# Performance work log

Measured on AMD Instinct MI355X. Metric: run time of the kernel, lower is better.

The kernel has to match this reference:

```python
import jax, jax.numpy as jnp
import numpy as np

HIDDEN = 1024
NUM_HEADS = 16
HEAD = HIDDEN // NUM_HEADS  # 64
LEFT = 64
RIGHT = 8
NUM_POS = LEFT + RIGHT + 1  # 73


def setup_inputs() -> dict:
    key = jax.random.key(0)
    ks = jax.random.split(key, 10)
    s = 1.0 / np.sqrt(HIDDEN)
    return {
        "hidden_states": jax.random.normal(ks[0], (4, 2048, HIDDEN), jnp.float32),
        "Wq": jax.random.normal(ks[1], (HIDDEN, HIDDEN), jnp.float32) * s,
        "bq": jax.random.normal(ks[2], (HIDDEN,), jnp.float32) * 0.01,
        "Wk": jax.random.normal(ks[3], (HIDDEN, HIDDEN), jnp.float32) * s,
        "bk": jax.random.normal(ks[4], (HIDDEN,), jnp.float32) * 0.01,
        "Wv": jax.random.normal(ks[5], (HIDDEN, HIDDEN), jnp.float32) * s,
        "bv": jax.random.normal(ks[6], (HIDDEN,), jnp.float32) * 0.01,
        "Wo": jax.random.normal(ks[7], (HIDDEN, HIDDEN), jnp.float32) * s,
        "bo": jax.random.normal(ks[8], (HIDDEN,), jnp.float32) * 0.01,
        "dist_emb": jax.random.normal(ks[9], (NUM_POS, HEAD), jnp.float32),
    }


def reference(hidden_states, Wq, bq, Wk, bk, Wv, bv, Wo, bo, dist_emb):
    B, L, H = hidden_states.shape
    scale = 1.0 / np.sqrt(HEAD)
    # projections (torch Linear: x @ W.T + b), reshape to [B, nH, L, d]
    def proj(W, b):
        return (hidden_states @ W.T + b).reshape(B, L, NUM_HEADS, HEAD).transpose(0, 2, 1, 3)
    q = proj(Wq, bq)
    k = proj(Wk, bk)
    v = proj(Wv, bv)
    attn = jnp.einsum('bhld,bhrd->bhlr', q, k) * scale  # [B,H,L,L]
    # relative-key positional bias
    dist = jnp.arange(L)[None, :] - jnp.arange(L)[:, None]  # r - l
    dist = jnp.clip(dist, -LEFT, RIGHT) + LEFT  # indices in [0, NUM_POS)
    pos_emb = dist_emb[dist]  # [L, L, d]
    rel = jnp.einsum('bhld,lrd->bhlr', q, pos_emb) * scale
    attn = jax.nn.softmax(attn + rel, axis=-1)
    out = jnp.einsum('bhlr,bhrd->bhld', attn, v)
    out = out.transpose(0, 2, 1, 3).reshape(B, L, H)
    return out @ Wo.T + bo
```

## Files before the change

kernel.cpp:

```cpp
#include <hip/hip_runtime.h>
#include <stdint.h>

#define SEQ   2048
#define BATCH 4
#define NH    16
#define HD    64
#define HID   1024
#define NPOS  73

typedef __attribute__((ext_vector_type(8))) short short8;
typedef __attribute__((ext_vector_type(4))) short short4v;
typedef __attribute__((ext_vector_type(4))) float f32x4;

static __device__ __forceinline__ float bf2f(short s) {
  return __uint_as_float(((unsigned)(unsigned short)s) << 16);
}
static __device__ __forceinline__ short f2bf(float f) {
  unsigned u = __float_as_uint(f);
  u += 0x7fffu + ((u >> 16) & 1u);
  return (short)(u >> 16);
}
static __device__ __forceinline__ unsigned pkbf(float a, float b) {
  unsigned d;
  asm("v_cvt_pk_bf16_f32 %0, %1, %2" : "=v"(d) : "v"(a), "v"(b));
  return d;
}

static __device__ __forceinline__ void gload_lds16(const void* g, void* lds) {
  __builtin_amdgcn_global_load_lds(
      (const __attribute__((address_space(1))) unsigned int*)g,
      (__attribute__((address_space(3))) unsigned int*)lds, 16, 0, 0);
}

__global__ __launch_bounds__(256) void cvt_kernel(const float* __restrict__ in,
                                                  short* __restrict__ out, int n4) {
  int i = blockIdx.x * 256 + threadIdx.x;
  if (i >= n4) return;
  f32x4 f = *(const f32x4*)(in + (long)i * 4);
  short4v o;
  o[0] = f2bf(f[0]); o[1] = f2bf(f[1]); o[2] = f2bf(f[2]); o[3] = f2bf(f[3]);
  *(short4v*)(out + (long)i * 4) = o;
}

__global__ __launch_bounds__(256) void cvt4_kernel(const float* __restrict__ a,
                                                   const float* __restrict__ b,
                                                   const float* __restrict__ c,
                                                   const float* __restrict__ d,
                                                   short* __restrict__ oa,
                                                   short* __restrict__ ob,
                                                   short* __restrict__ oc,
                                                   short* __restrict__ od, int n4) {
  int i = blockIdx.x * 256 + threadIdx.x;
  if (i >= n4) return;
  int m = blockIdx.y;
  const float* in = m == 0 ? a : m == 1 ? b : m == 2 ? c : d;
  short* out = m == 0 ? oa : m == 1 ? ob : m == 2 ? oc : od;
  f32x4 f = *(const f32x4*)(in + (long)i * 4);
  short4v o;
  o[0] = f2bf(f[0]); o[1] = f2bf(f[1]); o[2] = f2bf(f[2]); o[3] = f2bf(f[3]);
  *(short4v*)(out + (long)i * 4) = o;
}

template <int MODE>
__global__ __launch_bounds__(256) void gemm_nt(const short* __restrict__ A,
                                               const short* __restrict__ B,
                                               const float* __restrict__ bias,
                                               void* __restrict__ Cout, float scale) {
  __shared__ __align__(16) short As[128 * 32];
  __shared__ __align__(16) short Bs[128 * 32];
  const int K = HID;
  const f32x4 fzero = {0.f, 0.f, 0.f, 0.f};
  int t = threadIdx.x;
  int w = t >> 6, lane = t & 63;
  int wr = w >> 1, wc = w & 1;
  int g = lane >> 4, r = lane & 15;
  long tile_m = (long)blockIdx.x * 128;
  long tile_n = (long)blockIdx.y * 128;

  f32x4 acc[4][4];
#pragma unroll
  for (int m = 0; m < 4; ++m)
#pragma unroll
    for (int n = 0; n < 4; ++n) acc[m][n] = fzero;

  int e0 = w * 1024 + lane * 8;
  int e1 = e0 + 512;
  const short* A0 = A + (tile_m + (e0 >> 5)) * K + (e0 & 31);
  const short* A1 = A + (tile_m + (e1 >> 5)) * K + (e1 & 31);
  const short* B0 = B + (tile_n + (e0 >> 5)) * K + (e0 & 31);
  const short* B1 = B + (tile_n + (e1 >> 5)) * K + (e1 & 31);

  for (int k0 = 0; k0 < K; k0 += 32) {
    __syncthreads();
    gload_lds16(A0 + k0, &As[e0]);
    gload_lds16(A1 + k0, &As[e1]);
    gload_lds16(B0 + k0, &Bs[e0]);
    gload_lds16(B1 + k0, &Bs[e1]);
    __syncthreads();
    short8 af[4], bfr[4];
#pragma unroll
    for (int m = 0; m < 4; ++m)
      af[m] = *(const short8*)&As[(wr * 64 + m * 16 + r) * 32 + g * 8];
#pragma unroll
    for (int n = 0; n < 4; ++n)
      bfr[n] = *(const short8*)&Bs[(wc * 64 + n * 16 + r) * 32 + g * 8];
#pragma unroll
    for (int m = 0; m < 4; ++m)
#pragma unroll
      for (int n = 0; n < 4; ++n)
        acc[m][n] = __builtin_amdgcn_mfma_f32_16x16x32_bf16(af[m], bfr[n], acc[m][n], 0, 0, 0);
  }

#pragma unroll
  for (int m = 0; m < 4; ++m) {
    int row0 = (int)tile_m + wr * 64 + m * 16 + g * 4;
#pragma unroll
    for (int n = 0; n < 4; ++n) {
      int col = (int)tile_n + wc * 64 + n * 16 + r;
      float bs = bias[col];
#pragma unroll
      for (int j = 0; j < 4; ++j) {
        int row = row0 + j;
        float val = (acc[m][n][j] + bs) * scale;
        if (MODE == 0) {
          int b = row >> 11, l = row & (SEQ - 1);
          int hh = col >> 6, d = col & 63;
          ((short*)Cout)[(((long)(b * NH + hh) * SEQ + l) << 6) + d] = f2bf(val);
        } else if (MODE == 2) {
          int b = row >> 11, l = row & (SEQ - 1);
          int hh = col >> 6, d = col & 63;
          ((short*)Cout)[(((long)(b * NH + hh) * HD + d) << 11) + l] = f2bf(val);
        } else {
          ((float*)Cout)[(long)row * HID + col] = val;
        }
      }
    }
  }
}

__global__ __launch_bounds__(256, 3) void attn_kernel(const short* __restrict__ Qg,
                                                      const short* __restrict__ Kg,
                                                      const short* __restrict__ Vg,
                                                      const short* __restrict__ DE,
                                                      short* __restrict__ ctx) {
  __shared__ __align__(16) char arena[32768];
  __shared__ __align__(16) short qd2[128 * NPOS];

  short* Qs = (short*)arena;
  short* Ds = (short*)(arena + 16384);

  const f32x4 fzero = {0.f, 0.f, 0.f, 0.f};
  int t = threadIdx.x;
  int w = t >> 6, lane = t & 63;
  int g = lane >> 4, r = lane & 15;
  int h = blockIdx.x & (NH - 1), b = blockIdx.x >> 4, qt = blockIdx.y;
  int q0 = qt * 128;
  const short* Qp = Qg + ((long)(b * NH + h) * SEQ + q0) * HD;
  const short* Kp = Kg + (long)(b * NH + h) * SEQ * HD;
  const short* VTp = Vg + (long)(b * NH + h) * HD * SEQ;

#pragma unroll
  for (int c = 0; c < 4; ++c)
    gload_lds16(Qp + c * 2048 + t * 8, &Qs[c * 2048 + t * 8]);
#pragma unroll
  for (int i = 0; i < 3; ++i) {
    int sl = i * 256 + t;
    if (sl < (NPOS * 64 / 8)) {
      int p = sl >> 3;
      int cc = ((sl & 7) ^ (p & 7)) * 8;
      gload_lds16(DE + p * 64 + cc, &Ds[sl * 8]);
    }
  }
  __syncthreads();

  for (int idx = t; idx < 128 * NPOS; idx += 256) {
    int row = idx / NPOS, p = idx - row * NPOS;
    int px = (p & 7) << 3;
    float acc = 0.f;
#pragma unroll
    for (int d0 = 0; d0 < 64; d0 += 8) {
      short8 a = *(const short8*)&Qs[row * 64 + d0];
      short8 bb = *(const short8*)&Ds[p * 64 + (d0 ^ px)];
#pragma unroll
      for (int j = 0; j < 8; ++j) acc += bf2f(a[j]) * bf2f(bb[j]);
    }
    qd2[idx] = f2bf(acc);
  }

  short8 aq[2][2];
#pragma unroll
  for (int hq = 0; hq < 2; ++hq)
#pragma unroll
    for (int kb = 0; kb < 2; ++kb)
      aq[hq][kb] = *(const short8*)&Qs[(w * 32 + hq * 16 + r) * 64 + kb * 32 + g * 8];
  __syncthreads();

  int qb0 = (w * 32 + r) * NPOS;
  int qb1 = qb0 + 16 * NPOS;
  float bl0 = bf2f(qd2[qb0]), br0 = bf2f(qd2[qb0 + 72]);
  float bl1 = bf2f(qd2[qb1]), br1 = bf2f(qd2[qb1 + 72]);

  int srow = lane >> 3;
  int ssl = ((lane & 7) ^ srow) * 8;
  const short* K0 = Kp + (long)(w * 16 + srow) * HD + ssl;
  const short* K1 = Kp + (long)(w * 16 + 8 + srow) * HD + ssl;
  const short* V0 = VTp + (long)(w * 16 + srow) * SEQ + ssl;
  const short* V1 = VTp + (long)(w * 16 + 8 + srow) * SEQ + ssl;
  int e0 = w * 1024 + lane * 8;
  int e1 = e0 + 512;
  int rx = (r & 7) << 3;
  int Lw = q0 + w * 32;

  {
    short* kb = (short*)arena;
    short* vb = kb + 4096;
    gload_lds16(K0, &kb[e0]);
    gload_lds16(K1, &kb[e1]);
    gload_lds16(V0, &vb[e0]);
    gload_lds16(V1, &vb[e1]);
  }
  __syncthreads();

  f32x4 o0[4], o1[4], lc0 = fzero, lc1 = fzero;
#pragma unroll
  for (int n = 0; n < 4; ++n) { o0[n] = fzero; o1[n] = fzero; }

  const short8 ones8 = {0x3F80, 0x3F80, 0x3F80, 0x3F80, 0x3F80, 0x3F80, 0x3F80, 0x3F80};
  union U8 { unsigned u[4]; short8 v; };

  for (int kt = 0; kt < 32; ++kt) {
    {
      int kvn = ((kt + 1) & 31) * 64;
      short* kb = (short*)(arena + (((kt + 1) & 1) << 14));
      short* vb = kb + 4096;
      gload_lds16(K0 + (long)kvn * HD, &kb[e0]);
      gload_lds16(K1 + (long)kvn * HD, &kb[e1]);
      gload_lds16(V0 + kvn, &vb[e0]);
      gload_lds16(V1 + kvn, &vb[e1]);
    }
    const short* Ks = (const short*)(arena + ((kt & 1) << 14));
    const short* Vt = Ks + 4096;
    int kv0 = kt * 64;

    f32x4 s0[4], s1[4];
#pragma unroll
    for (int n = 0; n < 4; ++n) { s0[n] = fzero; s1[n] = fzero; }
#pragma unroll
    for (int kb = 0; kb < 2; ++kb)
#pragma unroll
      for (int n = 0; n < 4; ++n) {
        short8 kfr = *(const short8*)&Ks[(n * 16 + r) * 64 + ((kb * 32 + g * 8) ^ rx)];
        s0[n] = __builtin_amdgcn_mfma_f32_16x16x32_bf16(kfr, aq[0][kb], s0[n], 0, 0, 0);
        s1[n] = __builtin_amdgcn_mfma_f32_16x16x32_bf16(kfr, aq[1][kb], s1[n], 0, 0, 0);
      }

    bool allL = (kv0 + 63) <= (Lw - 64);
    bool allR = kv0 >= (Lw + 31 + 8);
    if (allL || allR) {
      float b0 = allL ? bl0 : br0;
      float b1 = allL ? bl1 : br1;
#pragma unroll
      for (int n = 0; n < 4; ++n)
#pragma unroll
        for (int j = 0; j < 4; ++j) { s0[n][j] += b0; s1[n][j] += b1; }
    } else {
      int lq = q0 + w * 32 + r;
#pragma unroll
      for (int n = 0; n < 4; ++n) {
        int key = kv0 + n * 16 + g * 4;
#pragma unroll
        for (int j = 0; j < 4; ++j) {
          int d0i = key + j - lq;
          d0i = d0i < -64 ? -64 : (d0i > 8 ? 8 : d0i);
          int d1i = key + j - lq - 16;
          d1i = d1i < -64 ? -64 : (d1i > 8 ? 8 : d1i);
          s0[n][j] += bf2f(qd2[qb0 + d0i + 64]);
          s1[n][j] += bf2f(qd2[qb1 + d1i + 64]);
        }
      }
    }

#pragma unroll
    for (int n = 0; n < 4; ++n)
#pragma unroll
      for (int j = 0; j < 4; ++j) {
        s0[n][j] = __builtin_amdgcn_exp2f(s0[n][j]);
        s1[n][j] = __builtin_amdgcn_exp2f(s1[n][j]);
      }

#pragma unroll
    for (int w32 = 0; w32 < 2; ++w32) {
      U8 pb0, pb1;
      pb0.u[0] = pkbf(s0[2 * w32][0], s0[2 * w32][1]);
      pb0.u[1] = pkbf(s0[2 * w32][2], s0[2 * w32][3]);
      pb0.u[2] = pkbf(s0[2 * w32 + 1][0], s0[2 * w32 + 1][1]);
      pb0.u[3] = pkbf(s0[2 * w32 + 1][2], s0[2 * w32 + 1][3]);
      pb1.u[0] = pkbf(s1[2 * w32][0], s1[2 * w32][1]);
      pb1.u[1] = pkbf(s1[2 * w32][2], s1[2 * w32][3]);
      pb1.u[2] = pkbf(s1[2 * w32 + 1][0], s1[2 * w32 + 1][1]);
      pb1.u[3] = pkbf(s1[2 * w32 + 1][2], s1[2 * w32 + 1][3]);
      lc0 = __builtin_amdgcn_mfma_f32_16x16x32_bf16(ones8, pb0.v, lc0, 0, 0, 0);
      lc1 = __builtin_amdgcn_mfma_f32_16x16x32_bf16(ones8, pb1.v, lc1, 0, 0, 0);
      int cA = (((w32 * 4 + (g >> 1)) ^ (r & 7)) << 3) + ((g & 1) * 4);
      int cB = (((w32 * 4 + 2 + (g >> 1)) ^ (r & 7)) << 3) + ((g & 1) * 4);
#pragma unroll
      for (int n = 0; n < 4; ++n) {
        const short* vrow = &Vt[(n * 16 + r) * 64];
        short4v va_ = *(const short4v*)(vrow + cA);
        short4v vb_ = *(const short4v*)(vrow + cB);
        short8 v8;
        v8[0] = va_[0]; v8[1] = va_[1]; v8[2] = va_[2]; v8[3] = va_[3];
        v8[4] = vb_[0]; v8[5] = vb_[1]; v8[6] = vb_[2]; v8[7] = vb_[3];
        o0[n] = __builtin_amdgcn_mfma_f32_16x16x32_bf16(v8, pb0.v, o0[n], 0, 0, 0);
        o1[n] = __builtin_amdgcn_mfma_f32_16x16x32_bf16(v8, pb1.v, o1[n], 0, 0, 0);
      }
    }
    __syncthreads();
  }

  float inv0 = 1.f / lc0[0], inv1 = 1.f / lc1[0];
  long grow0 = (long)(b * SEQ + q0 + w * 32 + r);
  long grow1 = grow0 + 16;
#pragma unroll
  for (int n = 0; n < 4; ++n) {
    uint2 v0, v1;
    v0.x = pkbf(o0[n][0] * inv0, o0[n][1] * inv0);
    v0.y = pkbf(o0[n][2] * inv0, o0[n][3] * inv0);
    v1.x = pkbf(o1[n][0] * inv1, o1[n][1] * inv1);
    v1.y = pkbf(o1[n][2] * inv1, o1[n][3] * inv1);
    *(uint2*)&ctx[grow0 * HID + h * 64 + n * 16 + g * 4] = v0;
    *(uint2*)&ctx[grow1 * HID + h * 64 + n * 16 + g * 4] = v1;
  }
}

extern "C" void kernel_launch(void* const* d_in, const int* in_sizes, int n_in,
                              void* d_out, int out_size, void* d_ws, size_t ws_size,
                              hipStream_t stream) {
  if (n_in < 10) return;
  const float* hs = (const float*)d_in[0];
  const float* Wq = (const float*)d_in[1];
  const float* bq = (const float*)d_in[2];
  const float* Wk = (const float*)d_in[3];
  const float* bk = (const float*)d_in[4];
  const float* Wv = (const float*)d_in[5];
  const float* bv = (const float*)d_in[6];
  const float* Wo = (const float*)d_in[7];
  const float* bo = (const float*)d_in[8];
  const float* de = (const float*)d_in[9];

  char* ws = (char*)d_ws;
  size_t off = 0;
  auto alloc = [&](size_t bytes) {
    size_t o = off;
    off += (bytes + 255) & ~(size_t)255;
    return o;
  };
  const size_t ACT = (size_t)BATCH * SEQ * HID * 2;
  const size_t WMT = (size_t)HID * HID * 2;
  short* hB  = (short*)(ws + alloc(ACT));
  short* wqB = (short*)(ws + alloc(WMT));
  short* wkB = (short*)(ws + alloc(WMT));
  short* wvB = (short*)(ws + alloc(WMT));
  short* woB = (short*)(ws + alloc(WMT));
  short* deB = (short*)(ws + alloc((size_t)NPOS * HD * 2));
  short* qB  = (short*)(ws + alloc(ACT));
  short* kB  = (short*)(ws + alloc(ACT));
  short* vB  = (short*)(ws + alloc(ACT));
  short* ctxB = hB;

  {
    int n4 = BATCH * SEQ * HID / 4;
    cvt_kernel<<<dim3((n4 + 255) / 256), dim3(256), 0, stream>>>(hs, hB, n4);
  }
  {
    int n4 = HID * HID / 4;
    cvt4_kernel<<<dim3((n4 + 255) / 256, 4), dim3(256), 0, stream>>>(
        Wq, Wk, Wv, Wo, wqB, wkB, wvB, woB, n4);
  }
  {
    int n4 = NPOS * HD / 4;
    cvt_kernel<<<dim3((n4 + 255) / 256), dim3(256), 0, stream>>>(de, deB, n4);
  }

  const float QSCALE = 0.125f * 1.4426950408889634f;
  dim3 gg(BATCH * SEQ / 128, HID / 128), blk(256);
  gemm_nt<0><<<gg, blk, 0, stream>>>(hB, wqB, bq, qB, QSCALE);
  gemm_nt<0><<<gg, blk, 0, stream>>>(hB, wkB, bk, kB, 1.0f);
  gemm_nt<2><<<gg, blk, 0, stream>>>(hB, wvB, bv, vB, 1.0f);

  attn_kernel<<<dim3(NH * BATCH, SEQ / 128), blk, 0, stream>>>(qB, kB, vB, deB, ctxB);

  gemm_nt<1><<<gg, blk, 0, stream>>>(ctxB, woB, bo, d_out, 1.0f);
}
```

Baseline: 254.5 us.

## Compute Q·dist_emb bias table with MFMA in a separate kernel

Moves the per-query relative-position dot products (Q against the 73 distance embeddings) out of the attention kernel into a new kernel. The new kernel uses bf16 MFMA instead of scalar bf16-to-float FMA loops and writes the table to a global workspace. The attention kernel then reads bias values from global memory instead of from LDS. This removes the scalar prologue and about 18 KB of LDS per block, which may raise occupancy. In exchange it adds an extra launch, roughly 19 MB of global write and read traffic, and uncoalesced global gathers on the diagonal tiles.

```diff
diff --git a/kernel.cpp b/kernel.cpp
--- a/kernel.cpp
+++ b/kernel.cpp
@@ -138,16 +138,74 @@
   }
 }
 
+__global__ __launch_bounds__(256) void qd_kernel(const short* __restrict__ Q,
+                                                 const short* __restrict__ DE,
+                                                 short* __restrict__ qd) {
+  __shared__ __align__(16) short Qs[128 * 64];
+  __shared__ __align__(16) short Es[80 * 64];
+  const f32x4 fzero = {0.f, 0.f, 0.f, 0.f};
+  int t = threadIdx.x;
+  int w = t >> 6, lane = t & 63;
+  int g = lane >> 4, r = lane & 15;
+  const short* Qp = Q + (long)blockIdx.x * (128 * 64);
+
+#pragma unroll
+  for (int c = 0; c < 4; ++c)
+    gload_lds16(Qp + c * 2048 + t * 8, &Qs[c * 2048 + t * 8]);
+#pragma unroll
+  for (int i = 0; i < 3; ++i) {
+    int s = i * 256 + t;
+    if (s < 584) gload_lds16(DE + s * 8, &Es[s * 8]);
+  }
+  __syncthreads();
+
+  short8 af[2][2];
+#pragma unroll
+  for (int m = 0; m < 2; ++m)
+#pragma unroll
+    for (int kb = 0; kb < 2; ++kb)
+      af[m][kb] = *(const short8*)&Qs[(w * 32 + m * 16 + r) * 64 + kb * 32 + g * 8];
+
+  f32x4 acc[2][5];
+#pragma unroll
+  for (int m = 0; m < 2; ++m)
+#pragma unroll
+    for (int n = 0; n < 5; ++n) acc[m][n] = fzero;
+
+#pragma unroll
+  for (int kb = 0; kb < 2; ++kb)
+#pragma unroll
+    for (int n = 0; n < 5; ++n) {
+      short8 bfr = *(const short8*)&Es[(n * 16 + r) * 64 + kb * 32 + g * 8];
+#pragma unroll
+      for (int m = 0; m < 2; ++m)
+        acc[m][n] = __builtin_amdgcn_mfma_f32_16x16x32_bf16(af[m][kb], bfr, acc[m][n], 0, 0, 0);
+    }
+
+  int p = r;
+#pragma unroll
+  for (int m = 0; m < 2; ++m) {
+#pragma unroll
+    for (int n = 0; n < 5; ++n) {
+      int pp = n * 16 + p;
+      if (pp < NPOS) {
+#pragma unroll
+        for (int j = 0; j < 4; ++j) {
+          long row = (long)blockIdx.x * 128 + w * 32 + m * 16 + g * 4 + j;
+          qd[row * NPOS + pp] = f2bf(acc[m][n][j]);
+        }
+      }
+    }
+  }
+}
+
 __global__ __launch_bounds__(256, 3) void attn_kernel(const short* __restrict__ Qg,
                                                       const short* __restrict__ Kg,
                                                       const short* __restrict__ Vg,
-                                                      const short* __restrict__ DE,
+                                                      const short* __restrict__ qdG,
                                                       short* __restrict__ ctx) {
   __shared__ __align__(16) char arena[32768];
-  __shared__ __align__(16) short qd2[128 * NPOS];
-
   short* Qs = (short*)arena;
-  short* Ds = (short*)(arena + 16384);
 
   const f32x4 fzero = {0.f, 0.f, 0.f, 0.f};
   int t = threadIdx.x;
@@ -162,30 +220,7 @@
 #pragma unroll
   for (int c = 0; c < 4; ++c)
     gload_lds16(Qp + c * 2048 + t * 8, &Qs[c * 2048 + t * 8]);
-#pragma unroll
-  for (int i = 0; i < 3; ++i) {
-    int sl = i * 256 + t;
-    if (sl < (NPOS * 64 / 8)) {
-      int p = sl >> 3;
-      int cc = ((sl & 7) ^ (p & 7)) * 8;
-      gload_lds16(DE + p * 64 + cc, &Ds[sl * 8]);
-    }
-  }
   __syncthreads();
-
-  for (int idx = t; idx < 128 * NPOS; idx += 256) {
-    int row = idx / NPOS, p = idx - row * NPOS;
-    int px = (p & 7) << 3;
-    float acc = 0.f;
-#pragma unroll
-    for (int d0 = 0; d0 < 64; d0 += 8) {
-      short8 a = *(const short8*)&Qs[row * 64 + d0];
-      short8 bb = *(const short8*)&Ds[p * 64 + (d0 ^ px)];
-#pragma unroll
-      for (int j = 0; j < 8; ++j) acc += bf2f(a[j]) * bf2f(bb[j]);
-    }
-    qd2[idx] = f2bf(acc);
-  }
 
   short8 aq[2][2];
 #pragma unroll
@@ -195,10 +230,12 @@
       aq[hq][kb] = *(const short8*)&Qs[(w * 32 + hq * 16 + r) * 64 + kb * 32 + g * 8];
   __syncthreads();
 
-  int qb0 = (w * 32 + r) * NPOS;
-  int qb1 = qb0 + 16 * NPOS;
-  float bl0 = bf2f(qd2[qb0]), br0 = bf2f(qd2[qb0 + 72]);
-  float bl1 = bf2f(qd2[qb1]), br1 = bf2f(qd2[qb1 + 72]);
+  long qrow0 = (long)(b * NH + h) * SEQ + q0 + w * 32 + r;
+  long qrow1 = qrow0 + 16;
+  const short* qd0 = qdG + qrow0 * NPOS;
+  const short* qd1 = qdG + qrow1 * NPOS;
+  float bl0 = bf2f(qd0[0]), br0 = bf2f(qd0[72]);
+  float bl1 = bf2f(qd1[0]), br1 = bf2f(qd1[72]);
 
   int srow = lane >> 3;
   int ssl = ((lane & 7) ^ srow) * 8;
@@ -274,8 +311,8 @@
           d0i = d0i < -64 ? -64 : (d0i > 8 ? 8 : d0i);
           int d1i = key + j - lq - 16;
           d1i = d1i < -64 ? -64 : (d1i > 8 ? 8 : d1i);
-          s0[n][j] += bf2f(qd2[qb0 + d0i + 64]);
-          s1[n][j] += bf2f(qd2[qb1 + d1i + 64]);
+          s0[n][j] += bf2f(qd0[d0i + 64]);
+          s1[n][j] += bf2f(qd1[d1i + 64]);
         }
       }
     }
@@ -366,6 +403,7 @@
   short* qB  = (short*)(ws + alloc(ACT));
   short* kB  = (short*)(ws + alloc(ACT));
   short* vB  = (short*)(ws + alloc(ACT));
+  short* qdB = (short*)(ws + alloc((size_t)BATCH * NH * SEQ * NPOS * 2));
   short* ctxB = hB;
 
   {
@@ -388,7 +426,9 @@
   gemm_nt<0><<<gg, blk, 0, stream>>>(hB, wkB, bk, kB, 1.0f);
   gemm_nt<2><<<gg, blk, 0, stream>>>(hB, wvB, bv, vB, 1.0f);
 
-  attn_kernel<<<dim3(NH * BATCH, SEQ / 128), blk, 0, stream>>>(qB, kB, vB, deB, ctxB);
+  qd_kernel<<<dim3(BATCH * NH * SEQ / 128), blk, 0, stream>>>(qB, deB, qdB);
+
+  attn_kernel<<<dim3(NH * BATCH, SEQ / 128), blk, 0, stream>>>(qB, kB, vB, qdB, ctxB);
 
   gemm_nt<1><<<gg, blk, 0, stream>>>(ctxB, woB, bo, d_out, 1.0f);
 }
```

Result: faster. 226.5 us (-11.0%).
